# Optimization experiments

Measured on AMD Instinct MI355X. Metric: run time of the kernel, lower is better.

The kernel has to match this reference:

```python
import jax, jax.numpy as jnp
import numpy as np

B, NA, NB, D, NH, APO = 32, 128, 128, 512, 16, 128
VA, VB, SUP_BDIST = 64, 32, 8
INV_SQRT_2PI_FACT = (2.0 * np.pi) ** 0.5


def setup_inputs() -> dict:
    key = jax.random.key(0)
    ks = jax.random.split(key, 20)
    atoms = jax.random.randint(ks[0], (B, NA), 0, VA)
    chirals = jax.random.randint(ks[1], (B, NA), 0, 4)
    coordinates = jax.random.normal(ks[2], (B, NA, 3), dtype=jnp.float32) * 5.0
    bonds = jax.random.randint(ks[3], (B, NA, NA), 0, VB)
    i0 = jax.random.randint(ks[4], (B, NB), 0, NA)
    off = jax.random.randint(ks[5], (B, NB), 1, NA)
    i1 = (i0 + off) % NA  # guarantee distinct endpoints so one-hot sum <= 1
    bond_indices = jnp.stack([i0, i1], axis=-1)
    bond_values = jax.random.randint(ks[6], (B, NB), 0, VB)
    bdist = jax.random.randint(ks[7], (B, NA, NA), 0, SUP_BDIST)
    sc = 0.02
    # embedding tables; rows for padding_idx=0 zeroed like torch nn.Embedding
    atype_emb = (jax.random.normal(ks[8], (VA, D)) * sc).at[0].set(0.0)
    chiral_emb = (jax.random.normal(ks[9], (4, D)) * sc).at[0].set(0.0)
    apair_w_tab = jax.random.normal(ks[10], (VA * VA, APO)) * sc
    apair_b_tab = jax.random.normal(ks[11], (VA * VA, APO)) * sc
    means = jax.random.normal(ks[12], (APO,)) * 0.1
    stds = jnp.ones((APO,), jnp.float32) + jax.random.normal(ks[13], (APO,)) * 0.1
    bond_emb_tab = (jax.random.normal(ks[14], (VB, NH)) * sc).at[0].set(0.0)
    lin_W = jax.random.normal(ks[15], (APO, NH)) * (1.0 / np.sqrt(APO))
    lin_b = jax.random.normal(ks[16], (NH,)) * sc
    btype_tab = (jax.random.normal(ks[17], (VB, D)) * sc).at[0].set(0.0)
    bond_atom_tab = (jax.random.normal(ks[18], (VA, D)) * sc).at[0].set(0.0)
    ab_connect_tab = (jax.random.normal(ks[19], (2, NH)) * sc).at[0].set(0.0)
    return dict(atoms=atoms, chirals=chirals, coordinates=coordinates, bonds=bonds,
                bond_indices=bond_indices, bond_values=bond_values, bdist=bdist,
                atype_emb=atype_emb, chiral_emb=chiral_emb, apair_w_tab=apair_w_tab,
                apair_b_tab=apair_b_tab, means=means, stds=stds, bond_emb_tab=bond_emb_tab,
                lin_W=lin_W, lin_b=lin_b, btype_tab=btype_tab, bond_atom_tab=bond_atom_tab,
                ab_connect_tab=ab_connect_tab)


def reference(atoms, chirals, coordinates, bonds, bond_indices, bond_values, bdist,
              atype_emb, chiral_emb, apair_w_tab, apair_b_tab, means, stds,
              bond_emb_tab, lin_W, lin_b, btype_tab, bond_atom_tab, ab_connect_tab):
    batch, n_atom = atoms.shape
    n_bond = bond_values.shape[1]
    # --- node embeddings ---
    atoms_e = atype_emb[atoms] + chiral_emb[chirals]                 # [B,Na,D]
    bonds_e = btype_tab[bond_values]                                  # [B,Nb,D]
    a0 = jnp.take_along_axis(atoms, bond_indices[:, :, 0], axis=1)    # [B,Nb]
    a1 = jnp.take_along_axis(atoms, bond_indices[:, :, 1], axis=1)
    bonds_e = bonds_e + bond_atom_tab[a0] + bond_atom_tab[a1]
    atoms_emb = jnp.concatenate([atoms_e, bonds_e], axis=1).transpose(1, 0, 2)  # [Na+Nb,B,D]
    # --- pairwise distances + RBF-modulated pair features ---
    diff = coordinates[:, None, :, :] - coordinates[:, :, None, :]    # [B,Na,Na,3]
    distances = jnp.sqrt(jnp.sum(diff * diff, axis=-1))               # [B,Na,Na]
    pair_idx = atoms[:, None, :] * VA + atoms[:, :, None]             # [B,Na,Na]
    x = apair_w_tab[pair_idx] * distances[..., None] + apair_b_tab[pair_idx]  # [B,Na,Na,APO]
    s = jnp.abs(stds) + 1e-5
    x = jnp.exp(-0.5 * jnp.square((x - means) / s)) / (INV_SQRT_2PI_FACT * s)
    apairs = jnp.einsum('bijp,ph->bijh', x, lin_W) + lin_b + bond_emb_tab[bonds]  # [B,Na,Na,NH]
    # --- atom-bond connectivity block ---
    oh = (jax.nn.one_hot(bond_indices[:, :, 0], n_atom, dtype=jnp.int32)
          + jax.nn.one_hot(bond_indices[:, :, 1], n_atom, dtype=jnp.int32))      # [B,Nb,Na]
    oh = oh * (bond_values != 0).astype(jnp.int32)[..., None]
    abpairs = ab_connect_tab[oh]                                       # [B,Nb,Na,NH]
    top = jnp.concatenate([apairs, abpairs], axis=1)                   # [B,Na+Nb,Na,NH]
    right = jnp.concatenate([abpairs.transpose(0, 2, 1, 3),
                             jnp.zeros((batch, n_bond, n_bond, NH), apairs.dtype)], axis=1)
    apairs = jnp.concatenate([top, right], axis=2)                     # [B,L,L,NH]
    padding_mask = jnp.concatenate([atoms == 0, bond_values == 0], axis=1)  # [B,L]
    apairs = jnp.where(padding_mask[:, None, :, None], -jnp.inf, apairs)
    apairs = apairs.transpose(0, 3, 1, 2)                              # [B,NH,L,L]
    # --- extended bdist ---
    oh_d = oh * SUP_BDIST
    bdist_out = jnp.concatenate([
        jnp.concatenate([bdist, oh_d], axis=1),
        jnp.concatenate([oh_d.transpose(0, 2, 1),
                         jnp.zeros((batch, n_bond, n_bond), oh_d.dtype)], axis=1)], axis=2)
    return atoms_emb, apairs, bdist_out, padding_mask
```

## Files before the change

kernel.cpp:

```cpp
#include <hip/hip_runtime.h>
#include <hip/hip_fp16.h>
#include <math.h>

#define B_ 32
#define NA_ 128
#define NB_ 128
#define D_ 512
#define NH_ 16
#define APO_ 128
#define L_ 256
#define VA_ 64

#define NEG_BIG (-3.0e38f)

#define WSB_WBT  2048
#define WSB_WBF  8192
#define WSB_BBF  (8192 + (1 << 20))
#define WS_NEED_BYTES (8192 + (2 << 20))

typedef __attribute__((ext_vector_type(8))) _Float16 f16x8;
typedef __attribute__((ext_vector_type(4))) float f32x4;

#define TROW 136

__global__ __launch_bounds__(256) void k0_fold(
    const float* __restrict__ wtab, const float* __restrict__ btab,
    const float* __restrict__ means, const float* __restrict__ stds,
    const float* __restrict__ linW, char* __restrict__ wsb) {
    int t = blockIdx.x * 256 + threadIdx.x;
    int ai = t >> 13;
    int aj = (t >> 7) & 63;
    int p = t & (APO_ - 1);
    int src = (aj << 13) + (ai << 7) + p;
    float s = fabsf(stds[p]) + 1e-5f;
    float si = 1.0f / s;
    _Float16* wbf = (_Float16*)(wsb + WSB_WBF);
    _Float16* bbf = (_Float16*)(wsb + WSB_BBF);
    wbf[t] = (_Float16)(wtab[src] * si);
    bbf[t] = (_Float16)((btab[src] - means[p]) * si);
    if (blockIdx.x == 0) {
        _Float16* wbT = (_Float16*)(wsb + WSB_WBT);
        for (int q = threadIdx.x; q < NH_ * APO_; q += 256) {
            int h = q >> 7, pp = q & 127;
            float s2 = fabsf(stds[pp]) + 1e-5f;
            float cof = 0.39894228040143270f / s2;
            wbT[q] = (_Float16)(linW[pp * NH_ + h] * cof);
        }
    }
}

__global__ __launch_bounds__(256, 4) void k_mega(
    const int* __restrict__ atoms, const int* __restrict__ chirals,
    const float* __restrict__ coords, const int* __restrict__ bonds,
    const int* __restrict__ bond_idx, const int* __restrict__ bond_vals,
    const int* __restrict__ bdist,
    const float* __restrict__ atype, const float* __restrict__ chiral_t,
    const float* __restrict__ btype, const float* __restrict__ batom,
    const float* __restrict__ ab_tab, const float* __restrict__ linb,
    const float* __restrict__ bond_emb, const char* __restrict__ wsb,
    float* __restrict__ out0, float* __restrict__ out1,
    float* __restrict__ out2, float* __restrict__ out3) {
    __shared__ _Float16 tab[2][64 * TROW];
    float (*epi)[129] = (float (*)[129]) & tab[0][0];

    int b = blockIdx.x >> 8;
    int r = blockIdx.x & 255;
    int tid = threadIdx.x;

    if (r < NA_) {
        int i = r;
        int wave = tid >> 6;
        int lane = tid & 63;
        int col = lane & 15;
        int kg = lane >> 4;

        int ai = atoms[b * NA_ + i];

        const _Float16* gw = (const _Float16*)(wsb + WSB_WBF) + (size_t)ai * (64 * APO_);
        const _Float16* gb = (const _Float16*)(wsb + WSB_BBF) + (size_t)ai * (64 * APO_);
#pragma unroll
        for (int it = 0; it < 4; ++it) {
            int g = (it * 256 + tid) * 8;
            int row = g >> 7, off = g & 127;
            *(f16x8*)&tab[0][row * TROW + off] = *(const f16x8*)(gw + g);
            *(f16x8*)&tab[1][row * TROW + off] = *(const f16x8*)(gb + g);
        }

        int j2 = tid & 127;
        int hg = tid >> 7;
        int ajr2 = atoms[b * NA_ + j2];
        int bij2 = bonds[((size_t)b * NA_ + i) * NA_ + j2];
        const float4* ber4 = (const float4*)(bond_emb + (size_t)bij2 * NH_);
        float4 berA = ber4[hg * 2 + 0];
        float4 berB = ber4[hg * 2 + 1];

        float cx = coords[((size_t)b * NA_ + i) * 3 + 0];
        float cy = coords[((size_t)b * NA_ + i) * 3 + 1];
        float cz = coords[((size_t)b * NA_ + i) * 3 + 2];
        __half2 d2[2];
        int rowh[2];
#pragma unroll
        for (int tt = 0; tt < 2; ++tt) {
            int jA = (wave * 2 + tt) * 16 + col;
            int ajt = atoms[b * NA_ + jA];
            float dx = coords[((size_t)b * NA_ + jA) * 3 + 0] - cx;
            float dy = coords[((size_t)b * NA_ + jA) * 3 + 1] - cy;
            float dz = coords[((size_t)b * NA_ + jA) * 3 + 2] - cz;
            float dist = sqrtf(dx * dx + dy * dy + dz * dz);
            d2[tt] = __float2half2_rn(dist);
            rowh[tt] = ajt * TROW;
        }

        const _Float16* wbT = (const _Float16*)(wsb + WSB_WBT);
        f16x8 Bf[4];
#pragma unroll
        for (int ks = 0; ks < 4; ++ks)
            Bf[ks] = *(const f16x8*)(wbT + col * APO_ + ks * 32 + kg * 8);

        const __half2 KE2 = __float2half2_rn(-0.72134752044448170f);

        __syncthreads();

        f32x4 accv[2];
#pragma unroll
        for (int tt = 0; tt < 2; ++tt) {
            f32x4 acc = {0.f, 0.f, 0.f, 0.f};
#pragma unroll
            for (int ks = 0; ks < 4; ++ks) {
                f16x8 w8 = *(const f16x8*)&tab[0][rowh[tt] + ks * 32 + kg * 8];
                f16x8 b8 = *(const f16x8*)&tab[1][rowh[tt] + ks * 32 + kg * 8];
                const __half2* wh = (const __half2*)&w8;
                const __half2* bh = (const __half2*)&b8;
                f16x8 af;
                __half2* eh = (__half2*)&af;
#pragma unroll
                for (int q = 0; q < 4; ++q) {
                    __half2 xh = __hfma2(wh[q], d2[tt], bh[q]);
                    __half2 t2 = __hmul2(__hmul2(xh, xh), KE2);
                    eh[q] = h2exp2(t2);
                }
                acc = __builtin_amdgcn_mfma_f32_16x16x32_f16(af, Bf[ks], acc, 0, 0, 0);
            }
            accv[tt] = acc;
        }
        __syncthreads();

#pragma unroll
        for (int tt = 0; tt < 2; ++tt) {
            int jb = (wave * 2 + tt) * 16;
#pragma unroll
            for (int rr = 0; rr < 4; ++rr)
                epi[col][jb + kg * 4 + rr] = accv[tt][rr];
        }
        __syncthreads();

        float berx[8] = {berA.x, berA.y, berA.z, berA.w, berB.x, berB.y, berB.z, berB.w};
        bool maskj = (ajr2 == 0);
        float* opb = out1 + (size_t)b * NH_ * L_ * L_ + (size_t)(hg * 8) * (L_ * L_)
                   + (size_t)i * L_ + j2;
#pragma unroll
        for (int q = 0; q < 8; ++q) {
            int h = hg * 8 + q;
            float v = epi[h][j2] + linb[h] + berx[q];
            opb[(size_t)q * (L_ * L_)] = maskj ? NEG_BIG : v;
        }
    }

    int c = tid;

    {
        float2 v;
        if (r < NA_) {
            int a = atoms[b * NA_ + r];
            int ch = chirals[b * NA_ + r];
            float2 v1 = ((const float2*)(atype + (size_t)a * D_))[c];
            float2 v2 = ((const float2*)(chiral_t + (size_t)ch * D_))[c];
            v = make_float2(v1.x + v2.x, v1.y + v2.y);
        } else {
            int k = r - NA_;
            int bv = bond_vals[b * NB_ + k];
            int i0 = bond_idx[(b * NB_ + k) * 2 + 0];
            int i1 = bond_idx[(b * NB_ + k) * 2 + 1];
            int a0 = atoms[b * NA_ + i0];
            int a1 = atoms[b * NA_ + i1];
            float2 v1 = ((const float2*)(btype + (size_t)bv * D_))[c];
            float2 v2 = ((const float2*)(batom + (size_t)a0 * D_))[c];
            float2 v3 = ((const float2*)(batom + (size_t)a1 * D_))[c];
            v = make_float2(v1.x + v2.x + v3.x, v1.y + v2.y + v3.y);
        }
        ((float2*)(out0 + ((size_t)r * B_ + b) * D_))[c] = v;
    }

    {
        float v = 0.0f;
        if (r < NA_) {
            if (c < NA_) {
                v = (float)bdist[((size_t)b * NA_ + r) * NA_ + c];
            } else {
                int k = c - NA_;
                int bv = bond_vals[b * NB_ + k];
                int i0 = bond_idx[(b * NB_ + k) * 2 + 0];
                int i1 = bond_idx[(b * NB_ + k) * 2 + 1];
                v = (bv != 0 && (i0 == r || i1 == r)) ? 8.0f : 0.0f;
            }
        } else if (c < NA_) {
            int k = r - NA_;
            int bv = bond_vals[b * NB_ + k];
            int i0 = bond_idx[(b * NB_ + k) * 2 + 0];
            int i1 = bond_idx[(b * NB_ + k) * 2 + 1];
            v = (bv != 0 && (i0 == c || i1 == c)) ? 8.0f : 0.0f;
        }
        out2[((size_t)b * L_ + r) * L_ + c] = v;
    }

    if (r == 0) {
        bool m = (c < NA_) ? (atoms[b * NA_ + c] == 0)
                           : (bond_vals[b * NB_ + (c - NA_)] == 0);
        out3[b * L_ + c] = m ? 1.0f : 0.0f;
    }

    if (r >= NA_ || c >= NA_) {
        float ohv = 0.0f;
        bool mask;
        if (c < NA_) {
            int k = r - NA_;
            int bv = bond_vals[b * NB_ + k];
            int i0 = bond_idx[(b * NB_ + k) * 2 + 0];
            int i1 = bond_idx[(b * NB_ + k) * 2 + 1];
            ohv = (bv != 0 && (i0 == c || i1 == c)) ? 1.0f : 0.0f;
            mask = (atoms[b * NA_ + c] == 0);
        } else {
            int k = c - NA_;
            int bv = bond_vals[b * NB_ + k];
            mask = (bv == 0);
            if (r < NA_) {
                int i0 = bond_idx[(b * NB_ + k) * 2 + 0];
                int i1 = bond_idx[(b * NB_ + k) * 2 + 1];
                ohv = (bv != 0 && (i0 == r || i1 == r)) ? 1.0f : 0.0f;
            }
        }
        float* op = out1 + (size_t)b * NH_ * L_ * L_ + (size_t)r * L_ + c;
#pragma unroll
        for (int h = 0; h < NH_; ++h) {
            float v = mask ? NEG_BIG : ohv * ab_tab[NH_ + h];
            op[(size_t)h * (L_ * L_)] = v;
        }
    }
}

__global__ __launch_bounds__(128) void k2_pair(
    const int* __restrict__ atoms, const float* __restrict__ coords,
    const int* __restrict__ bonds, const float* __restrict__ wtab,
    const float* __restrict__ btab, const float* __restrict__ linW,
    const float* __restrict__ linb, const float* __restrict__ bond_emb,
    const float* __restrict__ means, const float* __restrict__ stds,
    float* __restrict__ out1) {
    int b = blockIdx.x >> 7;
    int i = blockIdx.x & (NA_ - 1);
    int j = threadIdx.x;
    int ai = atoms[b * NA_ + i];
    int aj = atoms[b * NA_ + j];
    float cx = coords[((size_t)b * NA_ + i) * 3 + 0];
    float cy = coords[((size_t)b * NA_ + i) * 3 + 1];
    float cz = coords[((size_t)b * NA_ + i) * 3 + 2];
    float dx = coords[((size_t)b * NA_ + j) * 3 + 0] - cx;
    float dy = coords[((size_t)b * NA_ + j) * 3 + 1] - cy;
    float dz = coords[((size_t)b * NA_ + j) * 3 + 2] - cz;
    float dist = sqrtf(dx * dx + dy * dy + dz * dz);
    int idx = aj * VA_ + ai;
    const float4* wrow = (const float4*)(wtab + (size_t)idx * APO_);
    const float4* brow = (const float4*)(btab + (size_t)idx * APO_);
    float acc[NH_];
#pragma unroll
    for (int h = 0; h < NH_; ++h) acc[h] = 0.0f;
    const float KE = -0.72134752044448170f;
    for (int pp = 0; pp < APO_ / 4; ++pp) {
        float4 w4 = wrow[pp];
        float4 b4 = brow[pp];
        const float* wq = (const float*)&w4;
        const float* bq = (const float*)&b4;
#pragma unroll
        for (int q = 0; q < 4; ++q) {
            int p = pp * 4 + q;
            float s = fabsf(stds[p]) + 1e-5f;
            float si = 1.0f / s;
            float xh = fmaf(wq[q] * si, dist, fmaf(bq[q], si, -means[p] * si));
            float g = si * 0.39894228040143270f * exp2f(KE * xh * xh);
            const float* Wr = linW + p * NH_;
#pragma unroll
            for (int h = 0; h < NH_; ++h) acc[h] = fmaf(g, Wr[h], acc[h]);
        }
    }
    int bij = bonds[((size_t)b * NA_ + i) * NA_ + j];
    bool maskj = (aj == 0);
    float* op = out1 + (size_t)b * NH_ * L_ * L_ + (size_t)i * L_ + j;
#pragma unroll
    for (int h = 0; h < NH_; ++h) {
        float v = acc[h] + linb[h] + bond_emb[(size_t)bij * NH_ + h];
        op[(size_t)h * (L_ * L_)] = maskj ? NEG_BIG : v;
    }
}

__global__ __launch_bounds__(256) void k_fill(
    const int* __restrict__ atoms, const int* __restrict__ chirals,
    const int* __restrict__ bond_idx, const int* __restrict__ bond_vals,
    const int* __restrict__ bdist,
    const float* __restrict__ atype, const float* __restrict__ chiral_t,
    const float* __restrict__ btype, const float* __restrict__ batom,
    const float* __restrict__ ab_tab,
    float* __restrict__ out0, float* __restrict__ out1,
    float* __restrict__ out2, float* __restrict__ out3) {
    int b = blockIdx.x >> 8;
    int r = blockIdx.x & 255;
    int c = threadIdx.x;
    {
        float2 v;
        if (r < NA_) {
            int a = atoms[b * NA_ + r];
            int ch = chirals[b * NA_ + r];
            float2 v1 = ((const float2*)(atype + (size_t)a * D_))[c];
            float2 v2 = ((const float2*)(chiral_t + (size_t)ch * D_))[c];
            v = make_float2(v1.x + v2.x, v1.y + v2.y);
        } else {
            int k = r - NA_;
            int bv = bond_vals[b * NB_ + k];
            int i0 = bond_idx[(b * NB_ + k) * 2 + 0];
            int i1 = bond_idx[(b * NB_ + k) * 2 + 1];
            int a0 = atoms[b * NA_ + i0];
            int a1 = atoms[b * NA_ + i1];
            float2 v1 = ((const float2*)(btype + (size_t)bv * D_))[c];
            float2 v2 = ((const float2*)(batom + (size_t)a0 * D_))[c];
            float2 v3 = ((const float2*)(batom + (size_t)a1 * D_))[c];
            v = make_float2(v1.x + v2.x + v3.x, v1.y + v2.y + v3.y);
        }
        ((float2*)(out0 + ((size_t)r * B_ + b) * D_))[c] = v;
    }
    {
        float v = 0.0f;
        if (r < NA_) {
            if (c < NA_) {
                v = (float)bdist[((size_t)b * NA_ + r) * NA_ + c];
            } else {
                int k = c - NA_;
                int bv = bond_vals[b * NB_ + k];
                int i0 = bond_idx[(b * NB_ + k) * 2 + 0];
                int i1 = bond_idx[(b * NB_ + k) * 2 + 1];
                v = (bv != 0 && (i0 == r || i1 == r)) ? 8.0f : 0.0f;
            }
        } else if (c < NA_) {
            int k = r - NA_;
            int bv = bond_vals[b * NB_ + k];
            int i0 = bond_idx[(b * NB_ + k) * 2 + 0];
            int i1 = bond_idx[(b * NB_ + k) * 2 + 1];
            v = (bv != 0 && (i0 == c || i1 == c)) ? 8.0f : 0.0f;
        }
        out2[((size_t)b * L_ + r) * L_ + c] = v;
    }
    if (r == 0) {
        bool m = (c < NA_) ? (atoms[b * NA_ + c] == 0)
                           : (bond_vals[b * NB_ + (c - NA_)] == 0);
        out3[b * L_ + c] = m ? 1.0f : 0.0f;
    }
    if (r >= NA_ || c >= NA_) {
        float ohv = 0.0f;
        bool mask;
        if (c < NA_) {
            int k = r - NA_;
            int bv = bond_vals[b * NB_ + k];
            int i0 = bond_idx[(b * NB_ + k) * 2 + 0];
            int i1 = bond_idx[(b * NB_ + k) * 2 + 1];
            ohv = (bv != 0 && (i0 == c || i1 == c)) ? 1.0f : 0.0f;
            mask = (atoms[b * NA_ + c] == 0);
        } else {
            int k = c - NA_;
            int bv = bond_vals[b * NB_ + k];
            mask = (bv == 0);
            if (r < NA_) {
                int i0 = bond_idx[(b * NB_ + k) * 2 + 0];
                int i1 = bond_idx[(b * NB_ + k) * 2 + 1];
                ohv = (bv != 0 && (i0 == r || i1 == r)) ? 1.0f : 0.0f;
            }
        }
        float* op = out1 + (size_t)b * NH_ * L_ * L_ + (size_t)r * L_ + c;
#pragma unroll
        for (int h = 0; h < NH_; ++h) {
            float v = mask ? NEG_BIG : ohv * ab_tab[NH_ + h];
            op[(size_t)h * (L_ * L_)] = v;
        }
    }
}

extern "C" void kernel_launch(void* const* d_in, const int* in_sizes, int n_in,
                              void* d_out, int out_size, void* d_ws, size_t ws_size,
                              hipStream_t stream) {
    const int*   atoms     = (const int*)d_in[0];
    const int*   chirals   = (const int*)d_in[1];
    const float* coords    = (const float*)d_in[2];
    const int*   bonds     = (const int*)d_in[3];
    const int*   bond_idx  = (const int*)d_in[4];
    const int*   bond_vals = (const int*)d_in[5];
    const int*   bdist     = (const int*)d_in[6];
    const float* atype     = (const float*)d_in[7];
    const float* chiral_t  = (const float*)d_in[8];
    const float* wtab      = (const float*)d_in[9];
    const float* btab      = (const float*)d_in[10];
    const float* means     = (const float*)d_in[11];
    const float* stds      = (const float*)d_in[12];
    const float* bond_emb  = (const float*)d_in[13];
    const float* linW      = (const float*)d_in[14];
    const float* linb      = (const float*)d_in[15];
    const float* btype     = (const float*)d_in[16];
    const float* batom     = (const float*)d_in[17];
    const float* ab_tab    = (const float*)d_in[18];

    float* out  = (float*)d_out;
    float* out0 = out;
    float* out1 = out0 + (size_t)L_ * B_ * D_;
    float* out2 = out1 + (size_t)B_ * NH_ * L_ * L_;
    float* out3 = out2 + (size_t)B_ * L_ * L_;
    char*  wsb  = (char*)d_ws;

    bool use_fold = ws_size >= (size_t)WS_NEED_BYTES;

    if (use_fold) {
        hipLaunchKernelGGL(k0_fold, dim3(VA_ * VA_ * APO_ / 256), dim3(256), 0, stream,
                           wtab, btab, means, stds, linW, wsb);
        hipLaunchKernelGGL(k_mega, dim3(B_ * L_), dim3(256), 0, stream,
                           atoms, chirals, coords, bonds, bond_idx, bond_vals, bdist,
                           atype, chiral_t, btype, batom, ab_tab, linb, bond_emb, wsb,
                           out0, out1, out2, out3);
    } else {
        hipLaunchKernelGGL(k2_pair, dim3(B_ * NA_), dim3(NA_), 0, stream,
                           atoms, coords, bonds, wtab, btab, linW, linb, bond_emb,
                           means, stds, out1);
        hipLaunchKernelGGL(k_fill, dim3(B_ * L_), dim3(256), 0, stream,
                           atoms, chirals, bond_idx, bond_vals, bdist,
                           atype, chiral_t, btype, batom, ab_tab,
                           out0, out1, out2, out3);
    }
}
```

Measured before the change: 51.25 us.

## Move non-atom apairs quadrants to dedicated per-head blocks with float4 stores

Writing the bond-related quadrants of the attention-bias output moves out of the per-row blocks, where each thread issued 16 strided scalar stores across head planes, into 512 extra blocks, one per (batch, head) plane. Each of these blocks writes its plane with row-contiguous float4 stores. The goal is coalesced, wide writes for this large output region instead of head-strided scalar traffic. In exchange the grid has more blocks, and the bond-row quadrant still does per-row scalar loads of the bond index data.

```diff
diff --git a/kernel.cpp b/kernel.cpp
--- a/kernel.cpp
+++ b/kernel.cpp
@@ -63,9 +63,76 @@
     __shared__ _Float16 tab[2][64 * TROW];
     float (*epi)[129] = (float (*)[129]) & tab[0][0];
 
+    int tid = threadIdx.x;
+
+    if (blockIdx.x >= B_ * L_) {
+        int idx = blockIdx.x - B_ * L_;
+        int pb = idx >> 4;
+        int h = idx & 15;
+        float abh = ab_tab[NH_ + h];
+        float* plane = out1 + ((size_t)pb * NH_ + h) * (L_ * L_);
+
+        {
+            int c = NA_ + ((tid & 31) << 2);
+            int k = c - NA_;
+            int4 bv4 = *(const int4*)(bond_vals + pb * NB_ + k);
+            int4 p01 = *(const int4*)(bond_idx + (pb * NB_ + k) * 2);
+            int4 p23 = *(const int4*)(bond_idx + (pb * NB_ + k) * 2 + 4);
+            int rbase = tid >> 5;
+#pragma unroll
+            for (int r0 = 0; r0 < NA_; r0 += 8) {
+                int rr = r0 + rbase;
+                float4 vv;
+                vv.x = bv4.x ? ((p01.x == rr || p01.y == rr) ? abh : 0.f) : NEG_BIG;
+                vv.y = bv4.y ? ((p01.z == rr || p01.w == rr) ? abh : 0.f) : NEG_BIG;
+                vv.z = bv4.z ? ((p23.x == rr || p23.y == rr) ? abh : 0.f) : NEG_BIG;
+                vv.w = bv4.w ? ((p23.z == rr || p23.w == rr) ? abh : 0.f) : NEG_BIG;
+                *(float4*)(plane + (size_t)rr * L_ + c) = vv;
+            }
+        }
+
+        {
+            int c = (tid & 63) << 2;
+            int rbase = tid >> 6;
+            float4 left_zero = make_float4(0.f, 0.f, 0.f, 0.f);
+            bool m0, m1, m2, m3;
+            if (c < NA_) {
+                int4 aj4 = *(const int4*)(atoms + pb * NA_ + c);
+                m0 = (aj4.x == 0); m1 = (aj4.y == 0); m2 = (aj4.z == 0); m3 = (aj4.w == 0);
+            } else {
+                int4 bv4 = *(const int4*)(bond_vals + pb * NB_ + (c - NA_));
+                m0 = (bv4.x == 0); m1 = (bv4.y == 0); m2 = (bv4.z == 0); m3 = (bv4.w == 0);
+            }
+            float4 br;
+            br.x = m0 ? NEG_BIG : 0.f; br.y = m1 ? NEG_BIG : 0.f;
+            br.z = m2 ? NEG_BIG : 0.f; br.w = m3 ? NEG_BIG : 0.f;
+#pragma unroll
+            for (int r0 = 0; r0 < NA_; r0 += 4) {
+                int rr = NA_ + r0 + rbase;
+                float4 vv;
+                if (c < NA_) {
+                    int k = rr - NA_;
+                    int bvr = bond_vals[pb * NB_ + k];
+                    int i0r = bond_idx[(pb * NB_ + k) * 2 + 0];
+                    int i1r = bond_idx[(pb * NB_ + k) * 2 + 1];
+                    float o0 = (bvr && (i0r == c + 0 || i1r == c + 0)) ? abh : 0.f;
+                    float o1 = (bvr && (i0r == c + 1 || i1r == c + 1)) ? abh : 0.f;
+                    float o2 = (bvr && (i0r == c + 2 || i1r == c + 2)) ? abh : 0.f;
+                    float o3 = (bvr && (i0r == c + 3 || i1r == c + 3)) ? abh : 0.f;
+                    vv.x = m0 ? NEG_BIG : o0; vv.y = m1 ? NEG_BIG : o1;
+                    vv.z = m2 ? NEG_BIG : o2; vv.w = m3 ? NEG_BIG : o3;
+                } else {
+                    vv = br;
+                }
+                *(float4*)(plane + (size_t)rr * L_ + c) = vv;
+            }
+            (void)left_zero;
+        }
+        return;
+    }
+
     int b = blockIdx.x >> 8;
     int r = blockIdx.x & 255;
-    int tid = threadIdx.x;
 
     if (r < NA_) {
         int i = r;
@@ -217,34 +284,6 @@
         bool m = (c < NA_) ? (atoms[b * NA_ + c] == 0)
                            : (bond_vals[b * NB_ + (c - NA_)] == 0);
         out3[b * L_ + c] = m ? 1.0f : 0.0f;
-    }
-
-    if (r >= NA_ || c >= NA_) {
-        float ohv = 0.0f;
-        bool mask;
-        if (c < NA_) {
-            int k = r - NA_;
-            int bv = bond_vals[b * NB_ + k];
-            int i0 = bond_idx[(b * NB_ + k) * 2 + 0];
-            int i1 = bond_idx[(b * NB_ + k) * 2 + 1];
-            ohv = (bv != 0 && (i0 == c || i1 == c)) ? 1.0f : 0.0f;
-            mask = (atoms[b * NA_ + c] == 0);
-        } else {
-            int k = c - NA_;
-            int bv = bond_vals[b * NB_ + k];
-            mask = (bv == 0);
-            if (r < NA_) {
-                int i0 = bond_idx[(b * NB_ + k) * 2 + 0];
-                int i1 = bond_idx[(b * NB_ + k) * 2 + 1];
-                ohv = (bv != 0 && (i0 == r || i1 == r)) ? 1.0f : 0.0f;
-            }
-        }
-        float* op = out1 + (size_t)b * NH_ * L_ * L_ + (size_t)r * L_ + c;
-#pragma unroll
-        for (int h = 0; h < NH_; ++h) {
-            float v = mask ? NEG_BIG : ohv * ab_tab[NH_ + h];
-            op[(size_t)h * (L_ * L_)] = v;
-        }
     }
 }
 
@@ -425,7 +464,7 @@
     if (use_fold) {
         hipLaunchKernelGGL(k0_fold, dim3(VA_ * VA_ * APO_ / 256), dim3(256), 0, stream,
                            wtab, btab, means, stds, linW, wsb);
-        hipLaunchKernelGGL(k_mega, dim3(B_ * L_), dim3(256), 0, stream,
+        hipLaunchKernelGGL(k_mega, dim3(B_ * L_ + B_ * NH_), dim3(256), 0, stream,
                            atoms, chirals, coords, bonds, bond_idx, bond_vals, bdist,
                            atype, chiral_t, btype, batom, ab_tab, linb, bond_emb, wsb,
                            out0, out1, out2, out3);
```

Result: slower. 54.40 us (+6.1%).
